# Optimization experiments

Hardware: AMD Instinct MI355X
Metric: run time of the kernel (lower is better)

Reference implementation:

```python
import jax, jax.numpy as jnp
import numpy as np

B, N, D, E = 16, 4096, 1024, 64
TOP_K = 2
ROUTING_FLOOR_BASE = 0.05
CAP_LOW, CAP_HIGH, T_MAX = 0.5, 0.6, 1000


def setup_inputs() -> dict:
    key = jax.random.key(0)
    k1, k2, k3 = jax.random.split(key, 3)
    tokens_B = jax.random.normal(k1, (B, N, D), dtype=jnp.float32)
    t = jax.random.randint(k2, (B,), 0, T_MAX, dtype=jnp.int32)
    W_g = jax.random.normal(k3, (E, D), dtype=jnp.float32) * (1.0 / np.sqrt(D))
    b_g = jnp.zeros((E,), dtype=jnp.float32)
    return {"tokens_B": tokens_B, "t": t, "W_g": W_g, "b_g": b_g}


def _apply_routing_floor(probs, floor):
    # interpolate toward uniform so each expert gets >= floor mass
    e = probs.shape[-1]
    if floor <= 0.0:
        return probs
    alpha = min(floor * e, 1.0)
    return (1.0 - alpha) * probs + alpha / e


def _hard_cap(probs, t):
    # cap(t) = cap_low + (cap_high + cap_low) * t/T_max  (faithful to source)
    t_norm = t.astype(probs.dtype) / T_MAX
    cap = (CAP_LOW + (CAP_HIGH + CAP_LOW) * t_norm)[:, None, None]  # (B,1,1)
    excess = jax.nn.relu(probs - cap)
    capped = probs - excess
    headroom = jax.nn.relu(cap - capped)
    headroom_sum = jnp.clip(headroom.sum(-1, keepdims=True), 1e-8)
    capped = capped + excess.sum(-1, keepdims=True) * (headroom / headroom_sum)
    # torch version runs under no_grad; use straight-through so gate still trains
    return probs + jax.lax.stop_gradient(capped - probs)


def _topk_mask(probs, k):
    vals, idx = jax.lax.top_k(probs, k)  # (B,N,k)
    onehot = jax.nn.one_hot(idx, probs.shape[-1], dtype=probs.dtype)  # (B,N,k,E)
    return jnp.einsum('bnk,bnke->bne', vals, onehot)


def reference(tokens_B, t, W_g, b_g):
    logits = jnp.einsum('bnd,ed->bne', tokens_B, W_g) + b_g  # (B,N,E)
    probs = jax.nn.softmax(logits, axis=-1)
    floor = min(ROUTING_FLOOR_BASE, 0.15 / max(E, 1))
    probs = _apply_routing_floor(probs, floor)
    capped = _hard_cap(probs, t)
    gates = _topk_mask(capped, TOP_K)  # sparse gate mask (B,N,E)
    return gates
```

## Files before the change

kernel.cpp:

```cpp
#include <hip/hip_runtime.h>
#include <hip/hip_bf16.h>

typedef __attribute__((ext_vector_type(8))) short short8;
typedef __attribute__((ext_vector_type(4))) short sh4;
typedef __attribute__((ext_vector_type(4))) float floatx4;

__device__ __forceinline__ bool better(float va, int ia, float vb, int ib) {
    return (va > vb) || (va == vb && ia < ib);
}
__device__ __forceinline__ bool betterd(double va, int ia, double vb, int ib) {
    return (va > vb) || (va == vb && ia < ib);
}

__device__ __forceinline__ short bf16_rn(float f) {
    __hip_bfloat16 h = __float2bfloat16(f);
    return *reinterpret_cast<short*>(&h);
}
__device__ __forceinline__ float bf16_up(short s) {
    return __uint_as_float(((unsigned)(unsigned short)s) << 16);
}

__device__ __forceinline__ void split8(float4 a, float4 b, short8& hi, short8& lo) {
    float v[8] = {a.x, a.y, a.z, a.w, b.x, b.y, b.z, b.w};
    #pragma unroll
    for (int i = 0; i < 8; ++i) {
        short h = bf16_rn(v[i]);
        hi[i] = h;
        lo[i] = bf16_rn(v[i] - bf16_up(h));
    }
}

#define MFMA(A, B, C) __builtin_amdgcn_mfma_f32_16x16x32_bf16((A), (B), (C), 0, 0, 0)

__device__ __forceinline__ void gload16(const void* g, void* l) {
    __builtin_amdgcn_global_load_lds(
        (const __attribute__((address_space(1))) void*)g,
        (__attribute__((address_space(3))) void*)l,
        16, 0, 0);
}

__global__ __launch_bounds__(256)
void wsplit_kernel(const float* __restrict__ Wg,
                   short* __restrict__ whi,
                   short* __restrict__ wlo)
{
    const int idx = blockIdx.x * 256 + threadIdx.x;
    const int c = idx >> 8;
    const int g = (idx >> 6) & 3;
    const int q = (idx >> 4) & 3;
    const int e = idx & 15;
    const float* src = Wg + (size_t)(g * 16 + e) * 1024 + c * 32 + q * 8;
    float4 v0 = reinterpret_cast<const float4*>(src)[0];
    float4 v1 = reinterpret_cast<const float4*>(src)[1];
    short8 hi, lo;
    split8(v0, v1, hi, lo);
    reinterpret_cast<short8*>(whi)[idx] = hi;
    reinterpret_cast<short8*>(wlo)[idx] = lo;
}

__global__ __launch_bounds__(256, 4)
void router_kernel(const float* __restrict__ tokens,
                   const int* __restrict__ tarr,
                   const float* __restrict__ bg,
                   float* __restrict__ out,
                   int* __restrict__ flagCount,
                   int* __restrict__ flagList,
                   int listCap,
                   const short* __restrict__ whi,
                   const short* __restrict__ wlo)
{
    __shared__ __align__(16) char smem[32768];
    const int WH_OFF = 8192, WL_OFF = 12288;

    const int lane = threadIdx.x & 63;
    const int wave = threadIdx.x >> 6;
    const int c16  = lane & 15;
    const int quad = lane >> 4;

    const int tokenBase = blockIdx.x * 64;

    const char* aS0 = (const char*)tokens
        + (size_t)(tokenBase + wave * 16 + c16) * 4096 + quad * 32;
    const char* hS = (const char*)whi + wave * 1024 + (size_t)lane * 16;
    const char* lS = (const char*)wlo + wave * 1024 + (size_t)lane * 16;

    floatx4 acc0 = {0.f, 0.f, 0.f, 0.f};
    floatx4 acc1 = acc0, acc2 = acc0, acc3 = acc0;

    const int aRd = wave * 2048 + lane * 16;
    const int wRd = lane * 16;

    {
        char* b = smem;
        gload16(aS0,      b + wave * 2048);
        gload16(aS0 + 16, b + wave * 2048 + 1024);
        gload16(hS, b + WH_OFF + wave * 1024);
        gload16(lS, b + WL_OFF + wave * 1024);
    }

    for (int c = 0; c < 32; ++c) {
        char* cur = smem + (c & 1) * 16384;
        char* nxt = smem + ((c & 1) ^ 1) * 16384;

        if (c < 31) {
            const int co = (c + 1) * 128;
            const int cw = (c + 1) * 4096;
            gload16(aS0 + co,      nxt + wave * 2048);
            gload16(aS0 + co + 16, nxt + wave * 2048 + 1024);
            gload16(hS + cw, nxt + WH_OFF + wave * 1024);
            gload16(lS + cw, nxt + WL_OFF + wave * 1024);
            asm volatile("s_waitcnt vmcnt(4)" ::: "memory");
        } else {
            asm volatile("s_waitcnt vmcnt(0)" ::: "memory");
        }
        __builtin_amdgcn_s_barrier();
        asm volatile("" ::: "memory");

        float4 a0 = *(const float4*)(cur + aRd);
        float4 a1 = *(const float4*)(cur + aRd + 1024);
        short8 h0 = *(const short8*)(cur + WH_OFF +    0 + wRd);
        short8 h1 = *(const short8*)(cur + WH_OFF + 1024 + wRd);
        short8 h2 = *(const short8*)(cur + WH_OFF + 2048 + wRd);
        short8 h3 = *(const short8*)(cur + WH_OFF + 3072 + wRd);
        short8 l0 = *(const short8*)(cur + WL_OFF +    0 + wRd);
        short8 l1 = *(const short8*)(cur + WL_OFF + 1024 + wRd);
        short8 l2 = *(const short8*)(cur + WL_OFF + 2048 + wRd);
        short8 l3 = *(const short8*)(cur + WL_OFF + 3072 + wRd);

        short8 ahi, alo;
        split8(a0, a1, ahi, alo);

        acc0 = MFMA(ahi, h0, acc0); acc0 = MFMA(alo, h0, acc0); acc0 = MFMA(ahi, l0, acc0);
        acc1 = MFMA(ahi, h1, acc1); acc1 = MFMA(alo, h1, acc1); acc1 = MFMA(ahi, l1, acc1);
        acc2 = MFMA(ahi, h2, acc2); acc2 = MFMA(alo, h2, acc2); acc2 = MFMA(ahi, l2, acc2);
        acc3 = MFMA(ahi, h3, acc3); acc3 = MFMA(alo, h3, acc3); acc3 = MFMA(ahi, l3, acc3);

        __builtin_amdgcn_s_barrier();
        asm volatile("" ::: "memory");
    }

    __syncthreads();

    float* gtile = reinterpret_cast<float*>(smem);

    const float b0f = bg[c16 +  0];
    const float b1f = bg[c16 + 16];
    const float b2f = bg[c16 + 32];
    const float b3f = bg[c16 + 48];

    const float tb  = (float)tarr[tokenBase >> 12];
    const float cap = 0.5f + 1.1f * (tb / 1000.0f);

    const float A1 = 0.85f;
    const float A2 = 0.15f / 64.0f;

    #pragma unroll
    for (int rr = 0; rr < 4; ++rr) {
        float l0 = acc0[rr] + b0f;
        float l1 = acc1[rr] + b1f;
        float l2 = acc2[rr] + b2f;
        float l3 = acc3[rr] + b3f;

        float mx = fmaxf(fmaxf(l0, l1), fmaxf(l2, l3));
        #pragma unroll
        for (int off = 8; off >= 1; off >>= 1)
            mx = fmaxf(mx, __shfl_xor(mx, off));

        float e0 = expf(l0 - mx), e1 = expf(l1 - mx);
        float e2 = expf(l2 - mx), e3 = expf(l3 - mx);
        float s = e0 + e1 + e2 + e3;
        #pragma unroll
        for (int off = 8; off >= 1; off >>= 1)
            s += __shfl_xor(s, off);
        float inv = 1.0f / s;

        float p0 = A1 * (e0 * inv) + A2;
        float p1 = A1 * (e1 * inv) + A2;
        float p2 = A1 * (e2 * inv) + A2;
        float p3 = A1 * (e3 * inv) + A2;

        float x0 = fmaxf(p0 - cap, 0.f), x1 = fmaxf(p1 - cap, 0.f);
        float x2 = fmaxf(p2 - cap, 0.f), x3 = fmaxf(p3 - cap, 0.f);
        float m0 = p0 - x0, m1 = p1 - x1, m2 = p2 - x2, m3 = p3 - x3;
        float h0 = fmaxf(cap - m0, 0.f), h1 = fmaxf(cap - m1, 0.f);
        float h2 = fmaxf(cap - m2, 0.f), h3 = fmaxf(cap - m3, 0.f);
        float sx = x0 + x1 + x2 + x3;
        float sh = h0 + h1 + h2 + h3;
        #pragma unroll
        for (int off = 8; off >= 1; off >>= 1) {
            sx += __shfl_xor(sx, off);
            sh += __shfl_xor(sh, off);
        }
        sh = fmaxf(sh, 1e-8f);
        float sc = sx / sh;
        float c0 = m0 + sc * h0;
        float c1 = m1 + sc * h1;
        float c2 = m2 + sc * h2;
        float c3 = m3 + sc * h3;

        const int iA = c16, iB = c16 + 16, iC = c16 + 32, iD = c16 + 48;
        float v1, v2; int j1, j2;
        if (better(c0, iA, c1, iB)) { v1 = c0; j1 = iA; v2 = c1; j2 = iB; }
        else                        { v1 = c1; j1 = iB; v2 = c0; j2 = iA; }
        if (better(c2, iC, v1, j1))      { v2 = v1; j2 = j1; v1 = c2; j1 = iC; }
        else if (better(c2, iC, v2, j2)) { v2 = c2; j2 = iC; }
        if (better(c3, iD, v1, j1))      { v2 = v1; j2 = j1; v1 = c3; j1 = iD; }
        else if (better(c3, iD, v2, j2)) { v2 = c3; j2 = iD; }

        #pragma unroll
        for (int off = 1; off < 16; off <<= 1) {
            float w1 = __shfl_xor(v1, off); int k1 = __shfl_xor(j1, off);
            float w2 = __shfl_xor(v2, off); int k2 = __shfl_xor(j2, off);
            if (better(w1, k1, v1, j1)) {
                if (better(v1, j1, w2, k2)) { v2 = v1; j2 = j1; }
                else                        { v2 = w2; j2 = k2; }
                v1 = w1; j1 = k1;
            } else if (better(w1, k1, v2, j2)) {
                v2 = w1; j2 = k1;
            }
        }

        float g0 = (iA == j1 || iA == j2) ? c0 : 0.f;
        float g1 = (iB == j1 || iB == j2) ? c1 : 0.f;
        float g2 = (iC == j1 || iC == j2) ? c2 : 0.f;
        float g3 = (iD == j1 || iD == j2) ? c3 : 0.f;

        float t0 = (iA == j1 || iA == j2) ? -3.0e38f : c0;
        float t1 = (iB == j1 || iB == j2) ? -3.0e38f : c1;
        float t2 = (iC == j1 || iC == j2) ? -3.0e38f : c2;
        float t3 = (iD == j1 || iD == j2) ? -3.0e38f : c3;
        float m3v = fmaxf(fmaxf(t0, t1), fmaxf(t2, t3));
        #pragma unroll
        for (int off = 8; off >= 1; off >>= 1)
            m3v = fmaxf(m3v, __shfl_xor(m3v, off));

        const int tl = wave * 16 + quad * 4 + rr;
        bool flag = ((v2 - m3v) < 1e-4f) || (sx > 0.0f);
        if (flag && c16 == 0) {
            int pos = atomicAdd(flagCount, 1);
            if (pos < listCap) flagList[pos] = tokenBase + tl;
        }

        gtile[tl * 64 + iA] = g0;
        gtile[tl * 64 + iB] = g1;
        gtile[tl * 64 + iC] = g2;
        gtile[tl * 64 + iD] = g3;
    }

    __syncthreads();

    const uint4* src = reinterpret_cast<const uint4*>(gtile);
    uint4* dst = reinterpret_cast<uint4*>(out + (size_t)tokenBase * 64);
    dst[threadIdx.x]       = src[threadIdx.x];
    dst[threadIdx.x + 256] = src[threadIdx.x + 256];
    dst[threadIdx.x + 512] = src[threadIdx.x + 512];
    dst[threadIdx.x + 768] = src[threadIdx.x + 768];
}

__global__ __launch_bounds__(256, 4)
void router_kernel_legacy(const float* __restrict__ tokens,
                          const int* __restrict__ tarr,
                          const float* __restrict__ Wg,
                          const float* __restrict__ bg,
                          float* __restrict__ out,
                          int* __restrict__ flagCount,
                          int* __restrict__ flagList,
                          int listCap)
{
    __shared__ __align__(16) float gtile[64 * 64];

    const int lane = threadIdx.x & 63;
    const int wave = threadIdx.x >> 6;
    const int c16  = lane & 15;
    const int quad = lane >> 4;

    const int tokenBase = blockIdx.x * 64;
    const int token     = tokenBase + wave * 16 + c16;

    const float4* ap = reinterpret_cast<const float4*>(tokens) + (size_t)token * 256 + quad * 2;
    const float4* wp0 = reinterpret_cast<const float4*>(Wg) + (size_t)(c16 +  0) * 256 + quad * 2;
    const float4* wp1 = reinterpret_cast<const float4*>(Wg) + (size_t)(c16 + 16) * 256 + quad * 2;
    const float4* wp2 = reinterpret_cast<const float4*>(Wg) + (size_t)(c16 + 32) * 256 + quad * 2;
    const float4* wp3 = reinterpret_cast<const float4*>(Wg) + (size_t)(c16 + 48) * 256 + quad * 2;

    floatx4 acc0 = {0.f, 0.f, 0.f, 0.f};
    floatx4 acc1 = acc0, acc2 = acc0, acc3 = acc0;

    for (int kb = 0; kb < 32; ++kb) {
        short8 ahi, alo;
        split8(ap[kb * 8], ap[kb * 8 + 1], ahi, alo);
        {
            short8 whi, wlo;
            split8(wp0[kb * 8], wp0[kb * 8 + 1], whi, wlo);
            acc0 = MFMA(ahi, whi, acc0);
            acc0 = MFMA(alo, whi, acc0);
            acc0 = MFMA(ahi, wlo, acc0);
        }
        {
            short8 whi, wlo;
            split8(wp1[kb * 8], wp1[kb * 8 + 1], whi, wlo);
            acc1 = MFMA(ahi, whi, acc1);
            acc1 = MFMA(alo, whi, acc1);
            acc1 = MFMA(ahi, wlo, acc1);
        }
        {
            short8 whi, wlo;
            split8(wp2[kb * 8], wp2[kb * 8 + 1], whi, wlo);
            acc2 = MFMA(ahi, whi, acc2);
            acc2 = MFMA(alo, whi, acc2);
            acc2 = MFMA(ahi, wlo, acc2);
        }
        {
            short8 whi, wlo;
            split8(wp3[kb * 8], wp3[kb * 8 + 1], whi, wlo);
            acc3 = MFMA(ahi, whi, acc3);
            acc3 = MFMA(alo, whi, acc3);
            acc3 = MFMA(ahi, wlo, acc3);
        }
    }

    const float b0f = bg[c16 +  0];
    const float b1f = bg[c16 + 16];
    const float b2f = bg[c16 + 32];
    const float b3f = bg[c16 + 48];

    const float tb  = (float)tarr[tokenBase >> 12];
    const float cap = 0.5f + 1.1f * (tb / 1000.0f);

    const float A1 = 0.85f;
    const float A2 = 0.15f / 64.0f;

    #pragma unroll
    for (int r = 0; r < 4; ++r) {
        float l0 = acc0[r] + b0f;
        float l1 = acc1[r] + b1f;
        float l2 = acc2[r] + b2f;
        float l3 = acc3[r] + b3f;

        float mx = fmaxf(fmaxf(l0, l1), fmaxf(l2, l3));
        #pragma unroll
        for (int off = 8; off >= 1; off >>= 1)
            mx = fmaxf(mx, __shfl_xor(mx, off));

        float e0 = expf(l0 - mx), e1 = expf(l1 - mx);
        float e2 = expf(l2 - mx), e3 = expf(l3 - mx);
        float s = e0 + e1 + e2 + e3;
        #pragma unroll
        for (int off = 8; off >= 1; off >>= 1)
            s += __shfl_xor(s, off);
        float inv = 1.0f / s;

        float p0 = A1 * (e0 * inv) + A2;
        float p1 = A1 * (e1 * inv) + A2;
        float p2 = A1 * (e2 * inv) + A2;
        float p3 = A1 * (e3 * inv) + A2;

        float x0 = fmaxf(p0 - cap, 0.f), x1 = fmaxf(p1 - cap, 0.f);
        float x2 = fmaxf(p2 - cap, 0.f), x3 = fmaxf(p3 - cap, 0.f);
        float m0 = p0 - x0, m1 = p1 - x1, m2 = p2 - x2, m3 = p3 - x3;
        float h0 = fmaxf(cap - m0, 0.f), h1 = fmaxf(cap - m1, 0.f);
        float h2 = fmaxf(cap - m2, 0.f), h3 = fmaxf(cap - m3, 0.f);
        float sx = x0 + x1 + x2 + x3;
        float sh = h0 + h1 + h2 + h3;
        #pragma unroll
        for (int off = 8; off >= 1; off >>= 1) {
            sx += __shfl_xor(sx, off);
            sh += __shfl_xor(sh, off);
        }
        sh = fmaxf(sh, 1e-8f);
        float sc = sx / sh;
        float c0 = m0 + sc * h0;
        float c1 = m1 + sc * h1;
        float c2 = m2 + sc * h2;
        float c3 = m3 + sc * h3;

        const int iA = c16, iB = c16 + 16, iC = c16 + 32, iD = c16 + 48;
        float v1, v2; int j1, j2;
        if (better(c0, iA, c1, iB)) { v1 = c0; j1 = iA; v2 = c1; j2 = iB; }
        else                        { v1 = c1; j1 = iB; v2 = c0; j2 = iA; }
        if (better(c2, iC, v1, j1))      { v2 = v1; j2 = j1; v1 = c2; j1 = iC; }
        else if (better(c2, iC, v2, j2)) { v2 = c2; j2 = iC; }
        if (better(c3, iD, v1, j1))      { v2 = v1; j2 = j1; v1 = c3; j1 = iD; }
        else if (better(c3, iD, v2, j2)) { v2 = c3; j2 = iD; }

        #pragma unroll
        for (int off = 1; off < 16; off <<= 1) {
            float w1 = __shfl_xor(v1, off); int k1 = __shfl_xor(j1, off);
            float w2 = __shfl_xor(v2, off); int k2 = __shfl_xor(j2, off);
            if (better(w1, k1, v1, j1)) {
                if (better(v1, j1, w2, k2)) { v2 = v1; j2 = j1; }
                else                        { v2 = w2; j2 = k2; }
                v1 = w1; j1 = k1;
            } else if (better(w1, k1, v2, j2)) {
                v2 = w1; j2 = k1;
            }
        }

        float g0 = (iA == j1 || iA == j2) ? c0 : 0.f;
        float g1 = (iB == j1 || iB == j2) ? c1 : 0.f;
        float g2 = (iC == j1 || iC == j2) ? c2 : 0.f;
        float g3 = (iD == j1 || iD == j2) ? c3 : 0.f;

        float t0 = (iA == j1 || iA == j2) ? -3.0e38f : c0;
        float t1 = (iB == j1 || iB == j2) ? -3.0e38f : c1;
        float t2 = (iC == j1 || iC == j2) ? -3.0e38f : c2;
        float t3 = (iD == j1 || iD == j2) ? -3.0e38f : c3;
        float m3v = fmaxf(fmaxf(t0, t1), fmaxf(t2, t3));
        #pragma unroll
        for (int off = 8; off >= 1; off >>= 1)
            m3v = fmaxf(m3v, __shfl_xor(m3v, off));

        const int tl = wave * 16 + quad * 4 + r;
        bool flag = ((v2 - m3v) < 1e-4f) || (sx > 0.0f);
        if (flag && c16 == 0) {
            int pos = atomicAdd(flagCount, 1);
            if (pos < listCap) flagList[pos] = tokenBase + tl;
        }

        gtile[tl * 64 + iA] = g0;
        gtile[tl * 64 + iB] = g1;
        gtile[tl * 64 + iC] = g2;
        gtile[tl * 64 + iD] = g3;
    }

    __syncthreads();

    const uint4* src = reinterpret_cast<const uint4*>(gtile);
    uint4* dst = reinterpret_cast<uint4*>(out + (size_t)tokenBase * 64);
    dst[threadIdx.x]       = src[threadIdx.x];
    dst[threadIdx.x + 256] = src[threadIdx.x + 256];
    dst[threadIdx.x + 512] = src[threadIdx.x + 512];
    dst[threadIdx.x + 768] = src[threadIdx.x + 768];
}

__global__ __launch_bounds__(256)
void repair_kernel(const float* __restrict__ tokens,
                   const int* __restrict__ tarr,
                   const float* __restrict__ Wg,
                   const float* __restrict__ bg,
                   float* __restrict__ out,
                   const int* __restrict__ cnt,
                   const int* __restrict__ list,
                   int listCap)
{
    __shared__ __align__(16) float atile[8][1024];
    __shared__ double red[256];
    int count = cnt[0];
    if (count > listCap) count = listCap;

    const int e    = threadIdx.x & 63;
    const int part = threadIdx.x >> 6;

    for (int base = blockIdx.x * 8; base < count; base += gridDim.x * 8) {
        const int n = min(8, count - base);

        #pragma unroll
        for (int t = 0; t < 8; ++t) {
            if (t < n) {
                const float4* src =
                    reinterpret_cast<const float4*>(tokens + (size_t)list[base + t] * 1024);
                reinterpret_cast<float4*>(atile[t])[threadIdx.x] = src[threadIdx.x];
            }
        }
        __syncthreads();

        double acc0 = 0.0, acc1 = 0.0, acc2 = 0.0, acc3 = 0.0;
        double acc4 = 0.0, acc5 = 0.0, acc6 = 0.0, acc7 = 0.0;
        const float* wrow = Wg + (size_t)e * 1024 + part * 256;
        const int ko = part * 256;
        for (int k = 0; k < 256; k += 4) {
            float4 wv = *reinterpret_cast<const float4*>(wrow + k);
            const double w0 = (double)wv.x, w1 = (double)wv.y;
            const double w2 = (double)wv.z, w3 = (double)wv.w;
            #define ACC(T, A)                                                   \
                A = fma((double)atile[T][ko + k    ], w0, A);                    \
                A = fma((double)atile[T][ko + k + 1], w1, A);                    \
                A = fma((double)atile[T][ko + k + 2], w2, A);                    \
                A = fma((double)atile[T][ko + k + 3], w3, A);
            ACC(0, acc0) ACC(1, acc1) ACC(2, acc2) ACC(3, acc3)
            ACC(4, acc4) ACC(5, acc5) ACC(6, acc6) ACC(7, acc7)
            #undef ACC
        }

        #pragma unroll
        for (int t = 0; t < 8; ++t) {
            if (t >= n) break;
            double accT = (t == 0) ? acc0 : (t == 1) ? acc1 : (t == 2) ? acc2 :
                          (t == 3) ? acc3 : (t == 4) ? acc4 : (t == 5) ? acc5 :
                          (t == 6) ? acc6 : acc7;
            red[threadIdx.x] = accT;
            __syncthreads();

            if (threadIdx.x < 64) {
                const int token = list[base + t];
                double l = ((red[e] + red[64 + e]) + (red[128 + e] + red[192 + e]))
                         + (double)bg[e];

                double mxv = l;
                #pragma unroll
                for (int off = 32; off >= 1; off >>= 1)
                    mxv = fmax(mxv, __shfl_xor(mxv, off));
                double ex = exp(l - mxv);
                double s = ex;
                #pragma unroll
                for (int off = 32; off >= 1; off >>= 1)
                    s += __shfl_xor(s, off);

                const double alpha = 0.15;
                double p = (1.0 - alpha) * (ex / s) + alpha / 64.0;

                double tb  = (double)tarr[token >> 12];
                double capv = 0.5 + (0.6 + 0.5) * (tb / 1000.0);
                double x = fmax(p - capv, 0.0);
                double m = p - x;
                double h = fmax(capv - m, 0.0);
                double sx = x, sh = h;
                #pragma unroll
                for (int off = 32; off >= 1; off >>= 1) {
                    sx += __shfl_xor(sx, off);
                    sh += __shfl_xor(sh, off);
                }
                sh = fmax(sh, 1e-8);
                double c = m + (sx / sh) * h;

                double v1 = c, v2 = -1.0e300;
                int j1 = e, j2 = 127;
                #pragma unroll
                for (int off = 1; off < 64; off <<= 1) {
                    double w1 = __shfl_xor(v1, off); int k1 = __shfl_xor(j1, off);
                    double w2 = __shfl_xor(v2, off); int k2 = __shfl_xor(j2, off);
                    if (betterd(w1, k1, v1, j1)) {
                        if (betterd(v1, j1, w2, k2)) { v2 = v1; j2 = j1; }
                        else                         { v2 = w2; j2 = k2; }
                        v1 = w1; j1 = k1;
                    } else if (betterd(w1, k1, v2, j2)) {
                        v2 = w1; j2 = k1;
                    }
                }

                float g = (e == j1 || e == j2) ? (float)c : 0.0f;
                out[(size_t)token * 64 + e] = g;
            }
            __syncthreads();
        }
    }
}

extern "C" void kernel_launch(void* const* d_in, const int* in_sizes, int n_in,
                              void* d_out, int out_size, void* d_ws, size_t ws_size,
                              hipStream_t stream) {
    const float* tokens = (const float*)d_in[0];
    const int*   t      = (const int*)d_in[1];
    const float* Wg     = (const float*)d_in[2];
    const float* bg     = (const float*)d_in[3];
    float*       outp   = (float*)d_out;

    int* wsI = (int*)d_ws;
    const long long wsInts = (long long)(ws_size / 4);

    const int  WHALF   = 32768;
    const long long listOff = 16 + 2LL * WHALF;
    long long cap = wsInts - listOff;
    if (cap > 65536) cap = 65536;

    hipMemsetAsync(d_ws, 0, 64, stream);

    if (cap >= 32768) {
        short* whi  = (short*)(wsI + 16);
        short* wlo  = (short*)(wsI + 16 + WHALF);
        int*   list = wsI + listOff;
        wsplit_kernel<<<dim3(32), dim3(256), 0, stream>>>(Wg, whi, wlo);
        router_kernel<<<dim3(65536 / 64), dim3(256), 0, stream>>>(
            tokens, t, bg, outp, wsI, list, (int)cap, whi, wlo);
        repair_kernel<<<dim3(256), dim3(256), 0, stream>>>(
            tokens, t, Wg, bg, outp, wsI, list, (int)cap);
    } else {
        long long cap2 = wsInts - 16;
        if (cap2 < 0) cap2 = 0;
        if (cap2 > 65536) cap2 = 65536;
        router_kernel_legacy<<<dim3(65536 / 64), dim3(256), 0, stream>>>(
            tokens, t, Wg, bg, outp, wsI, wsI + 16, (int)cap2);
        repair_kernel<<<dim3(256), dim3(256), 0, stream>>>(
            tokens, t, Wg, bg, outp, wsI, wsI + 16, (int)cap2);
    }
}
```

Measured before the change: 448.4 us.

## Load token activations straight to registers and stage only gate weights in LDS

Token activations now go directly from global memory into registers, prefetched two chunks ahead. Only the bf16 hi/lo weight splits still go through a double-buffered LDS stage. The main loop is unrolled by two with explicit ping-pong buffers, and the gate tile gets its own LDS array instead of aliasing the staging buffer. Launch bounds drop from 4 to 2, allowing more registers per thread for the extra in-flight activation registers, at the risk of lower occupancy.

```diff
diff --git a/kernel.cpp b/kernel.cpp
--- a/kernel.cpp
+++ b/kernel.cpp
@@ -58,7 +58,7 @@
     reinterpret_cast<short8*>(wlo)[idx] = lo;
 }
 
-__global__ __launch_bounds__(256, 4)
+__global__ __launch_bounds__(256, 2)
 void router_kernel(const float* __restrict__ tokens,
                    const int* __restrict__ tarr,
                    const float* __restrict__ bg,
@@ -69,8 +69,8 @@
                    const short* __restrict__ whi,
                    const short* __restrict__ wlo)
 {
-    __shared__ __align__(16) char smem[32768];
-    const int WH_OFF = 8192, WL_OFF = 12288;
+    __shared__ __align__(16) float gtile[64 * 64];
+    __shared__ __align__(16) char  wbuf[2][8192];
 
     const int lane = threadIdx.x & 63;
     const int wave = threadIdx.x >> 6;
@@ -78,70 +78,85 @@
     const int quad = lane >> 4;
 
     const int tokenBase = blockIdx.x * 64;
-
-    const char* aS0 = (const char*)tokens
-        + (size_t)(tokenBase + wave * 16 + c16) * 4096 + quad * 32;
+    const int token     = tokenBase + wave * 16 + c16;
+
+    const float4* ap = reinterpret_cast<const float4*>(tokens) + (size_t)token * 256 + quad * 2;
+
     const char* hS = (const char*)whi + wave * 1024 + (size_t)lane * 16;
     const char* lS = (const char*)wlo + wave * 1024 + (size_t)lane * 16;
+    char* wb0h = wbuf[0];
+    char* wb1h = wbuf[1];
+
+    const int wRd = lane * 16;
 
     floatx4 acc0 = {0.f, 0.f, 0.f, 0.f};
     floatx4 acc1 = acc0, acc2 = acc0, acc3 = acc0;
 
-    const int aRd = wave * 2048 + lane * 16;
-    const int wRd = lane * 16;
-
-    {
-        char* b = smem;
-        gload16(aS0,      b + wave * 2048);
-        gload16(aS0 + 16, b + wave * 2048 + 1024);
-        gload16(hS, b + WH_OFF + wave * 1024);
-        gload16(lS, b + WL_OFF + wave * 1024);
+#define STAGE_W(c, wb)  do {                                              \
+        gload16(hS + (size_t)(c) * 4096, (wb) + wave * 1024);             \
+        gload16(lS + (size_t)(c) * 4096, (wb) + 4096 + wave * 1024);      \
+    } while (0)
+
+#define LOAD_A(c, A0, A1)  do {                                           \
+        (A0) = ap[(c) * 8];                                               \
+        (A1) = ap[(c) * 8 + 1];                                           \
+    } while (0)
+
+#define COMPUTE(wb, A0, A1)  do {                                         \
+        const char* bW = (wb);                                            \
+        short8 h0 = *(const short8*)(bW +    0 + wRd);                    \
+        short8 h1 = *(const short8*)(bW + 1024 + wRd);                    \
+        short8 h2 = *(const short8*)(bW + 2048 + wRd);                    \
+        short8 h3 = *(const short8*)(bW + 3072 + wRd);                    \
+        short8 l0 = *(const short8*)(bW + 4096 + wRd);                    \
+        short8 l1 = *(const short8*)(bW + 5120 + wRd);                    \
+        short8 l2 = *(const short8*)(bW + 6144 + wRd);                    \
+        short8 l3 = *(const short8*)(bW + 7168 + wRd);                    \
+        short8 ahi, alo;                                                  \
+        split8((A0), (A1), ahi, alo);                                     \
+        acc0 = MFMA(ahi, h0, acc0); acc0 = MFMA(alo, h0, acc0); acc0 = MFMA(ahi, l0, acc0); \
+        acc1 = MFMA(ahi, h1, acc1); acc1 = MFMA(alo, h1, acc1); acc1 = MFMA(ahi, l1, acc1); \
+        acc2 = MFMA(ahi, h2, acc2); acc2 = MFMA(alo, h2, acc2); acc2 = MFMA(ahi, l2, acc2); \
+        acc3 = MFMA(ahi, h3, acc3); acc3 = MFMA(alo, h3, acc3); acc3 = MFMA(ahi, l3, acc3); \
+    } while (0)
+
+#define WAIT4  asm volatile("s_waitcnt vmcnt(4)" ::: "memory")
+#define WAIT0  asm volatile("s_waitcnt vmcnt(0)" ::: "memory")
+#define BAR    do { __builtin_amdgcn_s_barrier(); asm volatile("" ::: "memory"); } while (0)
+
+    float4 a0A, a1A, a0B, a1B;
+
+    STAGE_W(0, wb0h);  LOAD_A(0, a0A, a1A);
+    STAGE_W(1, wb1h);  LOAD_A(1, a0B, a1B);
+
+    #pragma unroll 1
+    for (int cc = 0; cc < 15; ++cc) {
+        const int c0 = 2 * cc;
+        WAIT4;
+        BAR;
+        COMPUTE(wb0h, a0A, a1A);
+        BAR;
+        STAGE_W(c0 + 2, wb0h);  LOAD_A(c0 + 2, a0A, a1A);
+        WAIT4;
+        BAR;
+        COMPUTE(wb1h, a0B, a1B);
+        BAR;
+        STAGE_W(c0 + 3, wb1h);  LOAD_A(c0 + 3, a0B, a1B);
     }
-
-    for (int c = 0; c < 32; ++c) {
-        char* cur = smem + (c & 1) * 16384;
-        char* nxt = smem + ((c & 1) ^ 1) * 16384;
-
-        if (c < 31) {
-            const int co = (c + 1) * 128;
-            const int cw = (c + 1) * 4096;
-            gload16(aS0 + co,      nxt + wave * 2048);
-            gload16(aS0 + co + 16, nxt + wave * 2048 + 1024);
-            gload16(hS + cw, nxt + WH_OFF + wave * 1024);
-            gload16(lS + cw, nxt + WL_OFF + wave * 1024);
-            asm volatile("s_waitcnt vmcnt(4)" ::: "memory");
-        } else {
-            asm volatile("s_waitcnt vmcnt(0)" ::: "memory");
-        }
-        __builtin_amdgcn_s_barrier();
-        asm volatile("" ::: "memory");
-
-        float4 a0 = *(const float4*)(cur + aRd);
-        float4 a1 = *(const float4*)(cur + aRd + 1024);
-        short8 h0 = *(const short8*)(cur + WH_OFF +    0 + wRd);
-        short8 h1 = *(const short8*)(cur + WH_OFF + 1024 + wRd);
-        short8 h2 = *(const short8*)(cur + WH_OFF + 2048 + wRd);
-        short8 h3 = *(const short8*)(cur + WH_OFF + 3072 + wRd);
-        short8 l0 = *(const short8*)(cur + WL_OFF +    0 + wRd);
-        short8 l1 = *(const short8*)(cur + WL_OFF + 1024 + wRd);
-        short8 l2 = *(const short8*)(cur + WL_OFF + 2048 + wRd);
-        short8 l3 = *(const short8*)(cur + WL_OFF + 3072 + wRd);
-
-        short8 ahi, alo;
-        split8(a0, a1, ahi, alo);
-
-        acc0 = MFMA(ahi, h0, acc0); acc0 = MFMA(alo, h0, acc0); acc0 = MFMA(ahi, l0, acc0);
-        acc1 = MFMA(ahi, h1, acc1); acc1 = MFMA(alo, h1, acc1); acc1 = MFMA(ahi, l1, acc1);
-        acc2 = MFMA(ahi, h2, acc2); acc2 = MFMA(alo, h2, acc2); acc2 = MFMA(ahi, l2, acc2);
-        acc3 = MFMA(ahi, h3, acc3); acc3 = MFMA(alo, h3, acc3); acc3 = MFMA(ahi, l3, acc3);
-
-        __builtin_amdgcn_s_barrier();
-        asm volatile("" ::: "memory");
-    }
-
-    __syncthreads();
-
-    float* gtile = reinterpret_cast<float*>(smem);
+    WAIT4;
+    BAR;
+    COMPUTE(wb0h, a0A, a1A);
+    BAR;
+    WAIT0;
+    BAR;
+    COMPUTE(wb1h, a0B, a1B);
+
+#undef STAGE_W
+#undef LOAD_A
+#undef COMPUTE
+#undef WAIT4
+#undef WAIT0
+#undef BAR
 
     const float b0f = bg[c16 +  0];
     const float b1f = bg[c16 + 16];
```

After: 448.2 us. About the same (-0.1%).
